# Kernel tuning notes

Hardware: AMD Instinct MI355X
Metric: run time of the kernel (lower is better)

## Reference

```python
import jax, jax.numpy as jnp
import numpy as np

N_FFT = 4096
HOP = 1024
MAX_FRAMES = 345  # 44100*8 // 1024 + 1
BATCH = 8


def _build_buffers():
    N = N_FFT
    half = N // 2
    n = np.arange(N)
    k = np.arange(half + 1)
    ang = 2.0 * np.pi * np.outer(k, n) / N
    # fourier_basis = [real(fft(eye)[:half+1]); imag(fft(eye)[:half+1])], W[k,n]=exp(-2pi i kn/N)
    F = np.vstack([np.cos(ang), -np.sin(ang)])  # [N+2, N], float64
    window = 0.5 - 0.5 * np.cos(2.0 * np.pi * n / N)  # periodic hann, max == 1.0
    # rows of F are mutually orthogonal -> pinv(F) = F.T @ diag(1/||row||^2) (zero rows -> 0)
    norms = np.sum(F ** 2, axis=1)
    inv_norm = np.where(norms > 1e-6, 1.0 / norms, 0.0)
    # inverse_basis = window * pinv(F * N/HOP).T * sqrt(N)   (normalized=True)
    scale = inv_norm * (HOP / N) * np.sqrt(N)
    inverse_basis = (window[None, :] * F * scale[:, None]).astype(np.float32)  # [N+2, N]
    # window_sum normalization buffer
    T = MAX_FRAMES
    n_len = N + HOP * (T - 1)
    win_sq = (window / np.abs(window).max()) ** 2
    window_sum = np.zeros(n_len, dtype=np.float64)
    for i in range(T):
        s = i * HOP
        window_sum[s:s + N] += win_sq
    window_sum_inv = (N / (window_sum * HOP + 1e-8)).astype(np.float32)  # [n_len]
    return jnp.asarray(inverse_basis), jnp.asarray(window_sum_inv)


def setup_inputs() -> dict:
    key = jax.random.key(0)
    k1, k2 = jax.random.split(key)
    real = jax.random.normal(k1, (BATCH, N_FFT // 2 + 1, MAX_FRAMES), dtype=jnp.float32)
    imag = jax.random.normal(k2, (BATCH, N_FFT // 2 + 1, MAX_FRAMES), dtype=jnp.float32)
    inverse_basis, window_sum_inv = _build_buffers()
    return {"real": real, "imag": imag, "inverse_basis": inverse_basis,
            "window_sum_inv": window_sum_inv, "length": 352800}


def reference(real, imag, inverse_basis, window_sum_inv, length):
    eps = jnp.finfo(real.dtype).eps
    magnitude = jnp.sqrt(real ** 2 + imag ** 2)
    phase = jnp.arctan2(imag, real + eps)
    # [B, N+2, T]
    complex_input = jnp.concatenate([magnitude * jnp.cos(phase),
                                     magnitude * jnp.sin(phase)], axis=1)
    # conv_transpose1d(stride=HOP) == per-frame IDFT matmul + overlap-add
    frames = jnp.einsum('bct,ck->btk', complex_input, inverse_basis)  # [B, T, N]
    B, T, K = frames.shape
    n_len = K + HOP * (T - 1)
    idx = (jnp.arange(T)[:, None] * HOP + jnp.arange(K)[None, :]).reshape(-1)
    sig = jnp.zeros((B, n_len), frames.dtype).at[:, idx].add(frames.reshape(B, -1))
    half = K // 2
    out = sig[:, half:] * window_sum_inv[half:n_len]  # [B, n_len - half]
    if length:
        pad = max(0, length - out.shape[-1])
        out = jnp.pad(out, ((0, 0), (0, pad)))[:, :length]
    return out
```

## Files before the change

kernel.cpp:

```cpp
#include <hip/hip_runtime.h>
#include <cstdint>
#include <cstddef>

#define B_SZ  8
#define C_IN  2049
#define T_FR  345
#define NFFT  4096
#define HOPSZ 1024
#define MFR   2760
#define NPAIR 173
#define TW    1.5339807878856412e-3f
#define TW256 2.4543692606170259e-2f
#define W_INT 2.6666666666484f

#define C8P   0.70710678118654752f
#define C16C  0.92387953251128676f
#define C16S  0.38268343236508977f

typedef float f4 __attribute__((ext_vector_type(4)));

__device__ __forceinline__ unsigned short f2b(float f) {
  union { float f; unsigned int u; } v; v.f = f;
  unsigned int r = v.u + 0x7fffu + ((v.u >> 16) & 1u);
  return (unsigned short)(r >> 16);
}
__device__ __forceinline__ float b2f(unsigned int h) {
  union { unsigned int u; float f; } v; v.u = h << 16;
  return v.f;
}

__global__ void trans(const float* __restrict__ re, const float* __restrict__ im,
                      unsigned int* __restrict__ spec) {
  __shared__ float tr[64][65];
  __shared__ float ti[64][65];
  const int tid  = threadIdx.x;
  const int bid  = blockIdx.x;
  const int b    = bid & 7;
  const int tile = bid >> 3;
  const int t0 = (tile % 6) * 64;
  const int c0 = (tile / 6) * 64;
#pragma unroll
  for (int pass = 0; pass < 16; ++pass) {
    int idx = pass * 256 + tid;
    int tt = idx & 63, cc = idx >> 6;
    int c = c0 + cc, t = t0 + tt;
    float rp = 0.f, ip = 0.f;
    if (c < C_IN && t < T_FR) {
      size_t off = ((size_t)b * C_IN + c) * T_FR + t;
      float r = re[off], i = im[off];
      float x  = r + 1.1920929e-7f;
      float r2 = r * r + i * i;
      float h2 = fmaxf(x * x + i * i, 1e-35f);
      float inv = __builtin_amdgcn_sqrtf(r2) * __builtin_amdgcn_rsqf(h2);
      rp = x * inv;
      ip = i * inv;
    }
    tr[cc][tt] = rp;
    ti[cc][tt] = ip;
  }
  __syncthreads();
#pragma unroll
  for (int pass = 0; pass < 16; ++pass) {
    int idx = pass * 256 + tid;
    int kk = idx & 63, tt = idx >> 6;
    int c = c0 + kk, t = t0 + tt;
    if (c < C_IN && t < T_FR) {
      size_t mrow = (size_t)b * T_FR + t;
      unsigned int pk = ((unsigned int)f2b(ti[kk][tt]) << 16) | f2b(tr[kk][tt]);
      spec[mrow * C_IN + c] = pk;
    }
  }
}

__device__ __forceinline__ void cmul(float& xr, float& xi, float cr, float ci) {
  float t = xr * cr - xi * ci;
  xi = xr * ci + xi * cr;
  xr = t;
}

__device__ __forceinline__ void idft16(float* zr, float* zi) {
  float vr[16], vi[16];
#pragma unroll
  for (int a0 = 0; a0 < 4; ++a0) {
    float z0r = zr[a0],      z0i = zi[a0];
    float z1r = zr[a0 + 4],  z1i = zi[a0 + 4];
    float z2r = zr[a0 + 8],  z2i = zi[a0 + 8];
    float z3r = zr[a0 + 12], z3i = zi[a0 + 12];
    float t0r = z0r + z2r, t0i = z0i + z2i;
    float t1r = z0r - z2r, t1i = z0i - z2i;
    float t2r = z1r + z3r, t2i = z1i + z3i;
    float t3r = z3i - z1i, t3i = z1r - z3r;
    vr[a0 * 4 + 0] = t0r + t2r; vi[a0 * 4 + 0] = t0i + t2i;
    vr[a0 * 4 + 1] = t1r + t3r; vi[a0 * 4 + 1] = t1i + t3i;
    vr[a0 * 4 + 2] = t0r - t2r; vi[a0 * 4 + 2] = t0i - t2i;
    vr[a0 * 4 + 3] = t1r - t3r; vi[a0 * 4 + 3] = t1i - t3i;
  }
  cmul(vr[5],  vi[5],  C16C, C16S);
  cmul(vr[6],  vi[6],  C8P,  C8P);
  cmul(vr[7],  vi[7],  C16S, C16C);
  cmul(vr[9],  vi[9],  C8P,  C8P);
  { float t = vr[10]; vr[10] = -vi[10]; vi[10] = t; }
  cmul(vr[11], vi[11], -C8P, C8P);
  cmul(vr[13], vi[13], C16S, C16C);
  cmul(vr[14], vi[14], -C8P, C8P);
  cmul(vr[15], vi[15], -C16C, -C16S);
#pragma unroll
  for (int m0 = 0; m0 < 4; ++m0) {
    float z0r = vr[0 + m0],  z0i = vi[0 + m0];
    float z1r = vr[4 + m0],  z1i = vi[4 + m0];
    float z2r = vr[8 + m0],  z2i = vi[8 + m0];
    float z3r = vr[12 + m0], z3i = vi[12 + m0];
    float t0r = z0r + z2r, t0i = z0i + z2i;
    float t1r = z0r - z2r, t1i = z0i - z2i;
    float t2r = z1r + z3r, t2i = z1i + z3i;
    float t3r = z3i - z1i, t3i = z1r - z3r;
    zr[m0 + 0]  = t0r + t2r; zi[m0 + 0]  = t0i + t2i;
    zr[m0 + 4]  = t1r + t3r; zi[m0 + 4]  = t1i + t3i;
    zr[m0 + 8]  = t0r - t2r; zi[m0 + 8]  = t0i - t2i;
    zr[m0 + 12] = t1r - t3r; zi[m0 + 12] = t1i - t3i;
  }
}

__device__ __forceinline__ void twiddle_chain(float* zr, float* zi, float step) {
  float sA, cA; __sincosf(step, &sA, &cA);
  float cr = cA, ci = sA;
  cmul(zr[1], zi[1], cr, ci);
#pragma unroll
  for (int q = 2; q < 16; ++q) {
    float nr = cr * cA - ci * sA;
    ci = cr * sA + ci * cA;
    cr = nr;
    cmul(zr[q], zi[q], cr, ci);
  }
}

__global__ __launch_bounds__(256, 4) void ifft_frames(const unsigned int* __restrict__ spec,
                                                      unsigned short* __restrict__ Fr) {
  __shared__ float LR[4352];
  __shared__ float LI[4352];
  const int tid = threadIdx.x;
  const int bid = blockIdx.x;
  const int b = bid & 7;
  const int j = bid >> 3;
  const int ta = b * T_FR + 2 * j;
  const bool hasb = (2 * j + 1) < T_FR;
  const unsigned int* spa = spec + (size_t)ta * C_IN;
  const unsigned int* spb = spa + C_IN;

  float zr[16], zi[16];
#pragma unroll
  for (int q = 0; q < 16; ++q) {
    int n = tid + 256 * q;
    int k = (n <= 2048) ? n : (4096 - n);
    unsigned int va = spa[k];
    unsigned int vb = hasb ? spb[k] : 0u;
    float ar = b2f(va & 0xffffu), ai = b2f(va >> 16);
    float br = b2f(vb & 0xffffu), bi = b2f(vb >> 16);
    bool dc  = (n == 0) | (n == 2048);
    bool mir = n > 2048;
    float zzr = mir ? (ar + bi) : (ar - bi);
    float zzi = mir ? (br - ai) : (ai + br);
    zr[q] = dc ? ar : zzr;
    zi[q] = dc ? br : zzi;
  }
  idft16(zr, zi);
  {
    int base = (tid >> 4) + 17 * (tid & 15);
#pragma unroll
    for (int m = 0; m < 16; ++m) { LR[base + 272 * m] = zr[m]; LI[base + 272 * m] = zi[m]; }
  }
  __syncthreads();
  {
    int base = 17 * (tid & 15) + 272 * (tid >> 4);
#pragma unroll
    for (int q = 0; q < 16; ++q) { zr[q] = LR[base + q]; zi[q] = LI[base + q]; }
  }
  __syncthreads();
  twiddle_chain(zr, zi, (float)(tid >> 4) * TW256);
  idft16(zr, zi);
  {
    int base = (tid & 15) + 17 * (tid >> 4);
#pragma unroll
    for (int m = 0; m < 16; ++m) { LR[base + 272 * m] = zr[m]; LI[base + 272 * m] = zi[m]; }
  }
  __syncthreads();
  {
    int base = 17 * (tid & 15) + 272 * (tid >> 4);
#pragma unroll
    for (int q = 0; q < 16; ++q) { zr[q] = LR[base + q]; zi[q] = LI[base + q]; }
  }
  twiddle_chain(zr, zi, (float)tid * TW);
  idft16(zr, zi);
  unsigned int* da = (unsigned int*)(Fr + (size_t)ta * NFFT);
  unsigned int* db = (unsigned int*)(Fr + (size_t)(ta + 1) * NFFT);
  const bool even = (tid & 1) == 0;
#pragma unroll
  for (int m = 0; m < 16; ++m) {
    int n = 256 * m + tid;
    float w = (0.5f - 0.5f * __cosf((float)n * TW)) * 0.00390625f;
    float va = zr[m] * w, vb = zi[m] * w;
    float xa = __shfl_xor(va, 1);
    float xb = __shfl_xor(vb, 1);
    unsigned int pa = ((unsigned int)f2b(xa) << 16) | f2b(va);
    unsigned int pb = ((unsigned int)f2b(vb) << 16) | f2b(xb);
    int dw = 128 * m + (tid >> 1);
    if (even)      da[dw] = pa;
    else if (hasb) db[dw] = pb;
  }
}

__global__ void ola(const unsigned short* __restrict__ Fr, const float* __restrict__ wsi,
                    float* __restrict__ out, int length) {
  const int bid = blockIdx.x;
  const int b = bid & 7;
  const int pblk = bid >> 3;
  int q = pblk * 256 + threadIdx.x;
  int p4 = q * 4;
  if (p4 >= length) return;
  int s0 = (NFFT / 2) + p4;
  int tlo = (s0 - 3072) >> 10;
  tlo = tlo < 0 ? 0 : tlo;
  int thi = s0 >> 10;
  thi = thi > (T_FR - 1) ? (T_FR - 1) : thi;
  float a0 = 0.f, a1 = 0.f, a2 = 0.f, a3 = 0.f;
  for (int t = tlo; t <= thi; ++t) {
    const unsigned short* fp = Fr + ((size_t)(b * T_FR + t)) * NFFT + (s0 - (t << 10));
    ushort4 v = *(const ushort4*)fp;
    a0 += b2f(v.x); a1 += b2f(v.y); a2 += b2f(v.z); a3 += b2f(v.w);
  }
  float4 wv;
  if (s0 >= 3072 && s0 <= 353276) {
    wv.x = W_INT; wv.y = W_INT; wv.z = W_INT; wv.w = W_INT;
  } else {
    wv = *(const float4*)(wsi + s0);
  }
  float4 o; o.x = a0 * wv.x; o.y = a1 * wv.y; o.z = a2 * wv.z; o.w = a3 * wv.w;
  *(float4*)(out + (size_t)b * length + p4) = o;
}

extern "C" void kernel_launch(void* const* d_in, const int* in_sizes, int n_in,
                              void* d_out, int out_size, void* d_ws, size_t ws_size,
                              hipStream_t stream) {
  const float* re  = (const float*)d_in[0];
  const float* im  = (const float*)d_in[1];
  const float* wsi = (const float*)d_in[3];
  float* out = (float*)d_out;
  const int length = out_size / B_SZ;

  unsigned int*   spec = (unsigned int*)d_ws;
  unsigned short* Fr   = (unsigned short*)(spec + (size_t)MFR * C_IN);

  trans<<<dim3(8 * 198), 256, 0, stream>>>(re, im, spec);
  ifft_frames<<<dim3(8 * NPAIR), 256, 0, stream>>>(spec, Fr);
  ola<<<dim3(8 * 345), 256, 0, stream>>>(Fr, wsi, out, length);
}
```

Baseline: 168.7 us.

## Reorder trans/ifft block mapping and widen OLA to 8 outputs per thread

The transpose kernel now walks tiles channel-major, and the IFFT kernel processes frame pairs in reverse block order. Both are meant to improve cache locality between consecutive blocks and between kernels (the IFFT starts on the most recently written spectrum rows). The overlap-add kernel now produces 8 outputs per thread with a fixed unrolled 4-frame loop and two ushort4 loads, halving the grid size and removing the variable-bound loop. The interior window constant range is adjusted for 8-wide groups, and launch bounds are added.

```diff
diff --git a/kernel.cpp b/kernel.cpp
--- a/kernel.cpp
+++ b/kernel.cpp
@@ -17,8 +17,6 @@
 #define C16C  0.92387953251128676f
 #define C16S  0.38268343236508977f
 
-typedef float f4 __attribute__((ext_vector_type(4)));
-
 __device__ __forceinline__ unsigned short f2b(float f) {
   union { float f; unsigned int u; } v; v.f = f;
   unsigned int r = v.u + 0x7fffu + ((v.u >> 16) & 1u);
@@ -29,16 +27,17 @@
   return v.f;
 }
 
-__global__ void trans(const float* __restrict__ re, const float* __restrict__ im,
-                      unsigned int* __restrict__ spec) {
+__global__ __launch_bounds__(256) void trans(const float* __restrict__ re,
+                                             const float* __restrict__ im,
+                                             unsigned int* __restrict__ spec) {
   __shared__ float tr[64][65];
   __shared__ float ti[64][65];
   const int tid  = threadIdx.x;
   const int bid  = blockIdx.x;
   const int b    = bid & 7;
   const int tile = bid >> 3;
-  const int t0 = (tile % 6) * 64;
-  const int c0 = (tile / 6) * 64;
+  const int t0 = (tile / 33) * 64;
+  const int c0 = (tile % 33) * 64;
 #pragma unroll
   for (int pass = 0; pass < 16; ++pass) {
     int idx = pass * 256 + tid;
@@ -141,7 +140,7 @@
   const int tid = threadIdx.x;
   const int bid = blockIdx.x;
   const int b = bid & 7;
-  const int j = bid >> 3;
+  const int j = (NPAIR - 1) - (bid >> 3);
   const int ta = b * T_FR + 2 * j;
   const bool hasb = (2 * j + 1) < T_FR;
   const unsigned int* spa = spec + (size_t)ta * C_IN;
@@ -209,33 +208,44 @@
   }
 }
 
-__global__ void ola(const unsigned short* __restrict__ Fr, const float* __restrict__ wsi,
-                    float* __restrict__ out, int length) {
+__global__ __launch_bounds__(256) void ola(const unsigned short* __restrict__ Fr,
+                                           const float* __restrict__ wsi,
+                                           float* __restrict__ out, int length) {
   const int bid = blockIdx.x;
   const int b = bid & 7;
   const int pblk = bid >> 3;
   int q = pblk * 256 + threadIdx.x;
-  int p4 = q * 4;
-  if (p4 >= length) return;
-  int s0 = (NFFT / 2) + p4;
-  int tlo = (s0 - 3072) >> 10;
-  tlo = tlo < 0 ? 0 : tlo;
-  int thi = s0 >> 10;
-  thi = thi > (T_FR - 1) ? (T_FR - 1) : thi;
-  float a0 = 0.f, a1 = 0.f, a2 = 0.f, a3 = 0.f;
-  for (int t = tlo; t <= thi; ++t) {
-    const unsigned short* fp = Fr + ((size_t)(b * T_FR + t)) * NFFT + (s0 - (t << 10));
-    ushort4 v = *(const ushort4*)fp;
-    a0 += b2f(v.x); a1 += b2f(v.y); a2 += b2f(v.z); a3 += b2f(v.w);
-  }
-  float4 wv;
-  if (s0 >= 3072 && s0 <= 353276) {
-    wv.x = W_INT; wv.y = W_INT; wv.z = W_INT; wv.w = W_INT;
+  int p8 = q * 8;
+  if (p8 >= length) return;
+  int s0 = (NFFT / 2) + p8;
+  int t3 = s0 >> 10;
+  float a[8] = {0.f, 0.f, 0.f, 0.f, 0.f, 0.f, 0.f, 0.f};
+#pragma unroll
+  for (int d = 0; d < 4; ++d) {
+    int t = t3 - 3 + d;
+    if ((unsigned)t < (unsigned)T_FR) {
+      const unsigned short* fp = Fr + ((size_t)(b * T_FR + t)) * NFFT + (s0 - (t << 10));
+      const ushort4* fp4 = (const ushort4*)fp;
+      ushort4 v0 = fp4[0];
+      ushort4 v1 = fp4[1];
+      a[0] += b2f(v0.x); a[1] += b2f(v0.y); a[2] += b2f(v0.z); a[3] += b2f(v0.w);
+      a[4] += b2f(v1.x); a[5] += b2f(v1.y); a[6] += b2f(v1.z); a[7] += b2f(v1.w);
+    }
+  }
+  float4 w0, w1;
+  if (s0 >= 3072 && s0 <= 353272) {
+    w0.x = w0.y = w0.z = w0.w = W_INT;
+    w1 = w0;
   } else {
-    wv = *(const float4*)(wsi + s0);
-  }
-  float4 o; o.x = a0 * wv.x; o.y = a1 * wv.y; o.z = a2 * wv.z; o.w = a3 * wv.w;
-  *(float4*)(out + (size_t)b * length + p4) = o;
+    w0 = *(const float4*)(wsi + s0);
+    w1 = *(const float4*)(wsi + s0 + 4);
+  }
+  float* op = out + (size_t)b * length + p8;
+  float4 o0, o1;
+  o0.x = a[0] * w0.x; o0.y = a[1] * w0.y; o0.z = a[2] * w0.z; o0.w = a[3] * w0.w;
+  o1.x = a[4] * w1.x; o1.y = a[5] * w1.y; o1.z = a[6] * w1.z; o1.w = a[7] * w1.w;
+  *(float4*)(op)     = o0;
+  *(float4*)(op + 4) = o1;
 }
 
 extern "C" void kernel_launch(void* const* d_in, const int* in_sizes, int n_in,
@@ -252,5 +262,5 @@
 
   trans<<<dim3(8 * 198), 256, 0, stream>>>(re, im, spec);
   ifft_frames<<<dim3(8 * NPAIR), 256, 0, stream>>>(spec, Fr);
-  ola<<<dim3(8 * 345), 256, 0, stream>>>(Fr, wsi, out, length);
-}
+  ola<<<dim3(8 * 173), 256, 0, stream>>>(Fr, wsi, out, length);
+}
```

Result: no change. 167.5 us (-0.7%).
